# Optimization experiments

Measured on AMD Instinct MI355X. Metric: run time of the kernel, lower is better.

## Reference

```python
import jax, jax.numpy as jnp
import numpy as np

B, K, F_DIM, H_DIM, HEADS = 512, 17, 256, 256, 4
N = B * K           # 8704 flattened nodes
E = 139264          # edges (avg degree 16)
NEG_SLOPE = 0.2


def setup_inputs() -> dict:
    key = jax.random.key(0)
    ks = jax.random.split(key, 12)
    s_in = 1.0 / np.sqrt(F_DIM)
    s_hid = 1.0 / np.sqrt(H_DIM)
    return {
        "kpt_feature": jax.random.normal(ks[0], (B, K, F_DIM), jnp.float32),
        "edge_index": jax.random.randint(ks[1], (2, E), 0, N, jnp.int64),
        # conv1: F_DIM -> HEADS x H_DIM, concat=False (mean)
        "W1": jax.random.normal(ks[2], (F_DIM, HEADS * H_DIM), jnp.float32) * s_in,
        "a_src1": jax.random.normal(ks[3], (HEADS, H_DIM), jnp.float32) * s_hid,
        "a_dst1": jax.random.normal(ks[4], (HEADS, H_DIM), jnp.float32) * s_hid,
        "b1": jnp.zeros((H_DIM,), jnp.float32),
        # conv2: H_DIM -> HEADS x F_DIM, concat=False (mean)
        "W2": jax.random.normal(ks[5], (H_DIM, HEADS * F_DIM), jnp.float32) * s_hid,
        "a_src2": jax.random.normal(ks[6], (HEADS, F_DIM), jnp.float32) * s_in,
        "a_dst2": jax.random.normal(ks[7], (HEADS, F_DIM), jnp.float32) * s_in,
        "b2": jnp.zeros((F_DIM,), jnp.float32),
    }


def gat_conv(x, src, dst, W, a_src, a_dst, bias):
    # x: [N, Fin]; src/dst: [E'] (self-loops included); W: [Fin, H*C]
    n = x.shape[0]
    heads, c = a_src.shape
    h = (x @ W).reshape(n, heads, c)                       # [N,H,C]
    alpha_src = jnp.einsum("nhc,hc->nh", h, a_src)         # [N,H]
    alpha_dst = jnp.einsum("nhc,hc->nh", h, a_dst)
    e = jax.nn.leaky_relu(alpha_src[src] + alpha_dst[dst], NEG_SLOPE)  # [E',H]
    # segment softmax over incoming edges of each destination node
    emax = jax.ops.segment_max(e, dst, num_segments=n)
    emax = jnp.where(jnp.isfinite(emax), emax, 0.0)
    ex = jnp.exp(e - emax[dst])
    denom = jax.ops.segment_sum(ex, dst, num_segments=n)
    alpha = ex / denom[dst]                                # [E',H]
    msg = alpha[:, :, None] * h[src]                       # [E',H,C]
    out = jax.ops.segment_sum(msg, dst, num_segments=n)    # [N,H,C]
    return out.mean(axis=1) + bias                         # concat=False -> mean


def reference(kpt_feature, edge_index, W1, a_src1, a_dst1, b1, W2, a_src2, a_dst2, b2):
    b, k, f = kpt_feature.shape
    n = b * k
    x = kpt_feature.reshape(n, f)
    loop = jnp.arange(n, dtype=edge_index.dtype)
    src = jnp.concatenate([edge_index[0], loop])  # PyG add_self_loops=True
    dst = jnp.concatenate([edge_index[1], loop])
    x = gat_conv(x, src, dst, W1, a_src1, a_dst1, b1)
    x = jax.nn.relu(x)
    x = gat_conv(x, src, dst, W2, a_src2, a_dst2, b2)
    return x.reshape(b, k, f)
```

## Files before the change

### kernel.cpp

```cpp
#include <hip/hip_runtime.h>
#include <hip/hip_fp16.h>
#include <math.h>

#define NNODES 8704
#define NEDGE  139264
#define EPLUS  (NEDGE + NNODES)
#define NEG_SLOPE 0.2f
#define DEGCAP 64
#define LDSK   40

#define NB_PV  16
#define NB_WC  512
#define NB_SC  ((EPLUS + 255) / 256)
#define NB_AL  (NNODES / 4)

typedef _Float16 f16x8 __attribute__((ext_vector_type(8)));
typedef _Float16 f16x4 __attribute__((ext_vector_type(4)));
typedef float    f32x4 __attribute__((ext_vector_type(4)));

__device__ __forceinline__ float lrelu(float v) { return v >= 0.f ? v : NEG_SLOPE * v; }

__global__ __launch_bounds__(256) void prep_all(const float* __restrict__ W1,
                                                const float* __restrict__ as1,
                                                const float* __restrict__ ad1,
                                                const float* __restrict__ W2,
                                                const float* __restrict__ as2,
                                                const float* __restrict__ ad2,
                                                float* __restrict__ pbuf,
                                                int* __restrict__ cnt,
                                                float* __restrict__ alphasB,
                                                _Float16* __restrict__ Wc1,
                                                _Float16* __restrict__ Wc2) {
    __shared__ float tile[32][33];
    const int b = blockIdx.x;
    const int t = threadIdx.x;
    if (b < NB_PV) {
        for (int i = b * 256 + t; i < NNODES; i += NB_PV * 256) cnt[i] = 0;
        for (int i = b * 256 + t; i < NNODES * 8; i += NB_PV * 256) alphasB[i] = 0.f;
        float* a_sh = &tile[0][0];
        const int layer = b >> 3, sd = (b >> 2) & 1, h = b & 3;
        const float* W  = layer ? W2 : W1;
        const float* av = layer ? (sd ? ad2 : as2) : (sd ? ad1 : as1);
        a_sh[t] = av[h * 256 + t];
        __syncthreads();
        float acc = 0.f;
        const float* Wr = W + (size_t)t * 1024 + h * 256;
#pragma unroll 8
        for (int c = 0; c < 256; ++c) acc += Wr[c] * a_sh[c];
        pbuf[b * 256 + t] = acc;
    } else {
        const int idx = b - NB_PV;
        const int k0 = (idx & 7) * 32, o0 = ((idx >> 3) & 7) * 32;
        const int z = idx >> 6;
        const int layer = z >> 2, h = z & 3;
        const float* W = layer ? W2 : W1;
        _Float16* Wc   = layer ? Wc2 : Wc1;
#pragma unroll
        for (int p = 0; p < 4; ++p) {
            int e = t + p * 256; int kk = e >> 5, oo = e & 31;
            tile[kk][oo] = W[(size_t)(k0 + kk) * 1024 + h * 256 + o0 + oo];
        }
        __syncthreads();
#pragma unroll
        for (int p = 0; p < 4; ++p) {
            int e = t + p * 256; int oo = e >> 5, kk = e & 31;
            Wc[(size_t)(o0 + oo) * 1024 + h * 256 + k0 + kk] = (_Float16)tile[kk][oo];
        }
    }
}

__global__ __launch_bounds__(256) void scatter_alpha(const int* __restrict__ ei,
                                                     int* __restrict__ cnt,
                                                     int* __restrict__ csr,
                                                     const float* __restrict__ xf,
                                                     _Float16* __restrict__ xh_out,
                                                     const float* __restrict__ p ,
                                                     float* __restrict__ asrc,
                                                     float* __restrict__ adst) {
    const int b = blockIdx.x;
    const int t = threadIdx.x;
    if (b < NB_SC) {
        int e = b * 256 + t;
        if (e >= EPLUS) return;
        int src, dst;
        if (e < NEDGE) { src = ei[e]; dst = ei[NEDGE + e]; }
        else           { src = dst = e - NEDGE; }
        int slot = atomicAdd(&cnt[dst], 1);
        if (slot < DEGCAP) csr[dst * DEGCAP + slot] = src;
    } else {
        const int wave = t >> 6, l = t & 63;
        const int n = (b - NB_SC) * 4 + wave;
        float4 pv[8];
#pragma unroll
        for (int v = 0; v < 8; ++v) pv[v] = *(const float4*)(p + v * 256 + l * 4);
        float4 xv = *(const float4*)(xf + (size_t)n * 256 + l * 4);
        f16x4 hv = {(_Float16)xv.x, (_Float16)xv.y, (_Float16)xv.z, (_Float16)xv.w};
        *(f16x4*)(xh_out + (size_t)n * 256 + l * 4) = hv;
        float d[8];
#pragma unroll
        for (int v = 0; v < 8; ++v)
            d[v] = xv.x * pv[v].x + xv.y * pv[v].y + xv.z * pv[v].z + xv.w * pv[v].w;
#pragma unroll
        for (int off = 1; off <= 32; off <<= 1)
#pragma unroll
            for (int v = 0; v < 8; ++v) d[v] += __shfl_xor(d[v], off);
        if (l == 0) {
            *(float4*)(asrc + n * 4) = make_float4(d[0], d[1], d[2], d[3]);
            *(float4*)(adst + n * 4) = make_float4(d[4], d[5], d[6], d[7]);
        }
    }
}

__global__ __launch_bounds__(256) void agg_gather(const _Float16* __restrict__ xh,
                                                  const int* __restrict__ cnt,
                                                  const int* __restrict__ csr,
                                                  const float* __restrict__ asrc,
                                                  const float* __restrict__ adst,
                                                  _Float16* __restrict__ y) {
    const int w = threadIdx.x >> 6, l = threadIdx.x & 63;
    const int n = blockIdx.x * 4 + w;
    int deg = cnt[n]; if (deg > DEGCAP) deg = DEGCAP;

    float4 ad = *(const float4*)(adst + n * 4);
    int src_l = 0;
    float w0 = 0.f, w1 = 0.f, w2 = 0.f, w3 = 0.f;
    if (l < deg) {
        src_l = csr[n * DEGCAP + l];
        float4 as = *(const float4*)(asrc + src_l * 4);
        w0 = __expf(lrelu(as.x + ad.x));
        w1 = __expf(lrelu(as.y + ad.y));
        w2 = __expf(lrelu(as.z + ad.z));
        w3 = __expf(lrelu(as.w + ad.w));
    }
    float d0 = w0, d1 = w1, d2 = w2, d3 = w3;
#pragma unroll
    for (int off = 32; off >= 1; off >>= 1) {
        d0 += __shfl_xor(d0, off);
        d1 += __shfl_xor(d1, off);
        d2 += __shfl_xor(d2, off);
        d3 += __shfl_xor(d3, off);
    }
    w0 /= d0; w1 /= d1; w2 /= d2; w3 /= d3;

    float acc[4][4] = {};
    for (int s = 0; s < deg; ++s) {
        int src = __shfl(src_l, s);
        float u0 = __shfl(w0, s), u1 = __shfl(w1, s);
        float u2 = __shfl(w2, s), u3 = __shfl(w3, s);
        f16x4 xv = *(const f16x4*)(xh + (size_t)src * 256 + l * 4);
#pragma unroll
        for (int j = 0; j < 4; ++j) {
            float v = (float)xv[j];
            acc[j][0] += u0 * v; acc[j][1] += u1 * v;
            acc[j][2] += u2 * v; acc[j][3] += u3 * v;
        }
    }
#pragma unroll
    for (int h = 0; h < 4; ++h) {
        f16x4 pv = {(_Float16)acc[0][h], (_Float16)acc[1][h],
                    (_Float16)acc[2][h], (_Float16)acc[3][h]};
        *(f16x4*)(y + (size_t)n * 1024 + h * 256 + l * 4) = pv;
    }
}

__global__ __launch_bounds__(256) void gemm_out(const _Float16* __restrict__ Y,
                                                const _Float16* __restrict__ Wcatt,
                                                const float* __restrict__ bias,
                                                const float* __restrict__ p2,
                                                _Float16* __restrict__ outH,
                                                float* __restrict__ outF,
                                                float* __restrict__ asrc2,
                                                float* __restrict__ adst2) {
    __shared__ __align__(16) _Float16 As[64 * LDSK];
    __shared__ __align__(16) _Float16 Bs[256 * LDSK];
    __shared__ float p2s[8 * 256];
    const int t    = threadIdx.x;
    const int lane = t & 63;
    const int wave = t >> 6;
    const int wwr = wave >> 1, wwc = wave & 1;
    const int bm = blockIdx.x * 64;
    const int l15 = lane & 15, kb = lane >> 4;

    f32x4 acc[2][8] = {};

    int a_off[2], b_off[8];
#pragma unroll
    for (int i = 0; i < 2; ++i) a_off[i] = (wwr * 32 + i * 16 + l15) * LDSK + kb * 8;
#pragma unroll
    for (int j = 0; j < 8; ++j) b_off[j] = (wwc * 128 + j * 16 + l15) * LDSK + kb * 8;

    for (int k0 = 0; k0 < 1024; k0 += 32) {
        if (k0) __syncthreads();
        {
            int row = t >> 2, g = t & 3;
            f16x8 v = *(const f16x8*)(Y + (size_t)(bm + row) * 1024 + k0 + g * 8);
            *(f16x8*)(&As[row * LDSK + g * 8]) = v;
        }
#pragma unroll
        for (int p = 0; p < 4; ++p) {
            int e = t + p * 256;
            int row = e >> 2, g = e & 3;
            f16x8 v = *(const f16x8*)(Wcatt + (size_t)row * 1024 + k0 + g * 8);
            *(f16x8*)(&Bs[row * LDSK + g * 8]) = v;
        }
        __syncthreads();

        f16x8 af[2], bf[8];
#pragma unroll
        for (int i = 0; i < 2; ++i) af[i] = *(const f16x8*)(&As[a_off[i]]);
#pragma unroll
        for (int j = 0; j < 8; ++j) bf[j] = *(const f16x8*)(&Bs[b_off[j]]);
#pragma unroll
        for (int i = 0; i < 2; ++i)
#pragma unroll
            for (int j = 0; j < 8; ++j)
                acc[i][j] = __builtin_amdgcn_mfma_f32_16x16x32_f16(af[i], bf[j], acc[i][j], 0, 0, 0);
    }

    if (p2) {
#pragma unroll
        for (int v = 0; v < 8; ++v) p2s[v * 256 + t] = p2[v * 256 + t];
    }
    __syncthreads();

#pragma unroll
    for (int i = 0; i < 2; ++i)
#pragma unroll
        for (int q = 0; q < 4; ++q) {
            int row = bm + wwr * 32 + i * 16 + kb * 4 + q;
            float rv[8];
#pragma unroll
            for (int j = 0; j < 8; ++j) {
                int col = wwc * 128 + j * 16 + l15;
                float r = 0.25f * acc[i][j][q] + bias[col];
                rv[j] = r;
                if (outH) outH[(size_t)row * 256 + col] = (_Float16)fmaxf(r, 0.f);
                else      outF[(size_t)row * 256 + col] = r;
            }
            if (p2) {
#pragma unroll
                for (int v = 0; v < 8; ++v) {
                    float ps = 0.f;
#pragma unroll
                    for (int j = 0; j < 8; ++j) {
                        int col = wwc * 128 + j * 16 + l15;
                        ps += fmaxf(rv[j], 0.f) * p2s[v * 256 + col];
                    }
#pragma unroll
                    for (int off = 1; off <= 8; off <<= 1) ps += __shfl_xor(ps, off);
                    if (l15 == 0) {
                        if (v < 4) atomicAdd(&asrc2[row * 4 + v], ps);
                        else       atomicAdd(&adst2[row * 4 + (v - 4)], ps);
                    }
                }
            }
        }
}

extern "C" void kernel_launch(void* const* d_in, const int* in_sizes, int n_in,
                              void* d_out, int out_size, void* d_ws, size_t ws_size,
                              hipStream_t stream) {
    const float* x0  = (const float*)d_in[0];
    const int*   ei  = (const int*)d_in[1];
    const float* W1  = (const float*)d_in[2];
    const float* as1 = (const float*)d_in[3];
    const float* ad1 = (const float*)d_in[4];
    const float* b1  = (const float*)d_in[5];
    const float* W2  = (const float*)d_in[6];
    const float* as2 = (const float*)d_in[7];
    const float* ad2 = (const float*)d_in[8];
    const float* b2  = (const float*)d_in[9];
    float* out = (float*)d_out;

    char* w = (char*)d_ws;
    _Float16* y   = (_Float16*)w; w += (size_t)NNODES * 1024 * 2;
    _Float16* x0h = (_Float16*)w; w += (size_t)NNODES * 256 * 2;
    _Float16* x1h = (_Float16*)w; w += (size_t)NNODES * 256 * 2;
    _Float16* Wc1 = (_Float16*)w; w += (size_t)256 * 1024 * 2;
    _Float16* Wc2 = (_Float16*)w; w += (size_t)256 * 1024 * 2;
    float* pbuf   = (float*)w;    w += 16 * 256 * 4;
    float* asrcA  = (float*)w;    w += NNODES * 4 * 4;
    float* adstA  = (float*)w;    w += NNODES * 4 * 4;
    float* alphasB = (float*)w;   w += NNODES * 8 * 4;
    float* asrcB  = alphasB;
    float* adstB  = alphasB + NNODES * 4;
    int* cnt      = (int*)w;      w += NNODES * 4;
    int* csr      = (int*)w;      w += (size_t)NNODES * DEGCAP * 4;

    prep_all<<<NB_PV + NB_WC, 256, 0, stream>>>(W1, as1, ad1, W2, as2, ad2,
                                                pbuf, cnt, alphasB, Wc1, Wc2);
    scatter_alpha<<<NB_SC + NB_AL, 256, 0, stream>>>(ei, cnt, csr, x0, x0h, pbuf, asrcA, adstA);

    agg_gather<<<NNODES / 4, 256, 0, stream>>>(x0h, cnt, csr, asrcA, adstA, y);
    gemm_out<<<NNODES / 64, 256, 0, stream>>>(y, Wc1, b1, pbuf + 8 * 256, x1h, nullptr, asrcB, adstB);

    agg_gather<<<NNODES / 4, 256, 0, stream>>>(x1h, cnt, csr, asrcB, adstB, y);
    gemm_out<<<NNODES / 64, 256, 0, stream>>>(y, Wc2, b2, nullptr, nullptr, out, nullptr, nullptr);
}
```

Baseline: 142.3 us.

## Split output GEMM over column halves with 512-thread blocks and deeper K tile

The output GEMM grid gains a second dimension that splits the 256 output columns into two halves. Each block now runs 8 waves, and each wave computes a 32x32 tile instead of 32x128. The K step doubles to 64 with a padded LDS stride. The intent is to double block count (136 to 272) to fill more CUs and raise occupancy. The cost is that every Y tile is loaded twice and each wave gets less MFMA reuse per LDS load.

```diff
diff --git a/kernel.cpp b/kernel.cpp
--- a/kernel.cpp
+++ b/kernel.cpp
@@ -7,7 +7,7 @@
 #define EPLUS  (NEDGE + NNODES)
 #define NEG_SLOPE 0.2f
 #define DEGCAP 64
-#define LDSK   40
+#define LDSK2  72
 
 #define NB_PV  16
 #define NB_WC  512
@@ -163,7 +163,7 @@
     }
 }
 
-__global__ __launch_bounds__(256) void gemm_out(const _Float16* __restrict__ Y,
+__global__ __launch_bounds__(512) void gemm_out(const _Float16* __restrict__ Y,
                                                 const _Float16* __restrict__ Wcatt,
                                                 const float* __restrict__ bias,
                                                 const float* __restrict__ p2,
@@ -171,55 +171,63 @@
                                                 float* __restrict__ outF,
                                                 float* __restrict__ asrc2,
                                                 float* __restrict__ adst2) {
-    __shared__ __align__(16) _Float16 As[64 * LDSK];
-    __shared__ __align__(16) _Float16 Bs[256 * LDSK];
-    __shared__ float p2s[8 * 256];
+    __shared__ __align__(16) _Float16 As[64 * LDSK2];
+    __shared__ __align__(16) _Float16 Bs[128 * LDSK2];
+    __shared__ float p2s[8 * 128];
     const int t    = threadIdx.x;
     const int lane = t & 63;
     const int wave = t >> 6;
-    const int wwr = wave >> 1, wwc = wave & 1;
+    const int wwr = wave >> 2, wwc = wave & 3;
     const int bm = blockIdx.x * 64;
+    const int bn = blockIdx.y * 128;
     const int l15 = lane & 15, kb = lane >> 4;
 
-    f32x4 acc[2][8] = {};
-
-    int a_off[2], b_off[8];
-#pragma unroll
-    for (int i = 0; i < 2; ++i) a_off[i] = (wwr * 32 + i * 16 + l15) * LDSK + kb * 8;
-#pragma unroll
-    for (int j = 0; j < 8; ++j) b_off[j] = (wwc * 128 + j * 16 + l15) * LDSK + kb * 8;
-
-    for (int k0 = 0; k0 < 1024; k0 += 32) {
+    f32x4 acc[2][2] = {};
+
+    int a_off[2], b_off[2];
+#pragma unroll
+    for (int i = 0; i < 2; ++i) a_off[i] = (wwr * 32 + i * 16 + l15) * LDSK2 + kb * 8;
+#pragma unroll
+    for (int j = 0; j < 2; ++j) b_off[j] = (wwc * 32 + j * 16 + l15) * LDSK2 + kb * 8;
+
+    for (int k0 = 0; k0 < 1024; k0 += 64) {
         if (k0) __syncthreads();
         {
-            int row = t >> 2, g = t & 3;
+            int row = t >> 3, g = t & 7;
             f16x8 v = *(const f16x8*)(Y + (size_t)(bm + row) * 1024 + k0 + g * 8);
-            *(f16x8*)(&As[row * LDSK + g * 8]) = v;
-        }
-#pragma unroll
-        for (int p = 0; p < 4; ++p) {
-            int e = t + p * 256;
-            int row = e >> 2, g = e & 3;
-            f16x8 v = *(const f16x8*)(Wcatt + (size_t)row * 1024 + k0 + g * 8);
-            *(f16x8*)(&Bs[row * LDSK + g * 8]) = v;
+            *(f16x8*)(&As[row * LDSK2 + g * 8]) = v;
+        }
+#pragma unroll
+        for (int p = 0; p < 2; ++p) {
+            int e = t + p * 512;
+            int row = e >> 3, g = e & 7;
+            f16x8 v = *(const f16x8*)(Wcatt + (size_t)(bn + row) * 1024 + k0 + g * 8);
+            *(f16x8*)(&Bs[row * LDSK2 + g * 8]) = v;
         }
         __syncthreads();
 
-        f16x8 af[2], bf[8];
-#pragma unroll
-        for (int i = 0; i < 2; ++i) af[i] = *(const f16x8*)(&As[a_off[i]]);
-#pragma unroll
-        for (int j = 0; j < 8; ++j) bf[j] = *(const f16x8*)(&Bs[b_off[j]]);
-#pragma unroll
-        for (int i = 0; i < 2; ++i)
-#pragma unroll
-            for (int j = 0; j < 8; ++j)
-                acc[i][j] = __builtin_amdgcn_mfma_f32_16x16x32_f16(af[i], bf[j], acc[i][j], 0, 0, 0);
+#pragma unroll
+        for (int ks = 0; ks < 2; ++ks) {
+            f16x8 af[2], bf[2];
+#pragma unroll
+            for (int i = 0; i < 2; ++i) af[i] = *(const f16x8*)(&As[a_off[i] + ks * 32]);
+#pragma unroll
+            for (int j = 0; j < 2; ++j) bf[j] = *(const f16x8*)(&Bs[b_off[j] + ks * 32]);
+#pragma unroll
+            for (int i = 0; i < 2; ++i)
+#pragma unroll
+                for (int j = 0; j < 2; ++j)
+                    acc[i][j] = __builtin_amdgcn_mfma_f32_16x16x32_f16(af[i], bf[j], acc[i][j], 0, 0, 0);
+        }
     }
 
     if (p2) {
 #pragma unroll
-        for (int v = 0; v < 8; ++v) p2s[v * 256 + t] = p2[v * 256 + t];
+        for (int p = 0; p < 2; ++p) {
+            int e = t + p * 512;
+            int v = e >> 7, c = e & 127;
+            p2s[e] = p2[v * 256 + bn + c];
+        }
     }
     __syncthreads();
 
@@ -228,23 +236,23 @@
 #pragma unroll
         for (int q = 0; q < 4; ++q) {
             int row = bm + wwr * 32 + i * 16 + kb * 4 + q;
-            float rv[8];
-#pragma unroll
-            for (int j = 0; j < 8; ++j) {
-                int col = wwc * 128 + j * 16 + l15;
-                float r = 0.25f * acc[i][j][q] + bias[col];
+            float rv[2];
+#pragma unroll
+            for (int j = 0; j < 2; ++j) {
+                int cl = wwc * 32 + j * 16 + l15;
+                float r = 0.25f * acc[i][j][q] + bias[bn + cl];
                 rv[j] = r;
-                if (outH) outH[(size_t)row * 256 + col] = (_Float16)fmaxf(r, 0.f);
-                else      outF[(size_t)row * 256 + col] = r;
+                if (outH) outH[(size_t)row * 256 + bn + cl] = (_Float16)fmaxf(r, 0.f);
+                else      outF[(size_t)row * 256 + bn + cl] = r;
             }
             if (p2) {
 #pragma unroll
                 for (int v = 0; v < 8; ++v) {
                     float ps = 0.f;
 #pragma unroll
-                    for (int j = 0; j < 8; ++j) {
-                        int col = wwc * 128 + j * 16 + l15;
-                        ps += fmaxf(rv[j], 0.f) * p2s[v * 256 + col];
+                    for (int j = 0; j < 2; ++j) {
+                        int cl = wwc * 32 + j * 16 + l15;
+                        ps += fmaxf(rv[j], 0.f) * p2s[v * 128 + cl];
                     }
 #pragma unroll
                     for (int off = 1; off <= 8; off <<= 1) ps += __shfl_xor(ps, off);
@@ -287,13 +295,15 @@
     int* cnt      = (int*)w;      w += NNODES * 4;
     int* csr      = (int*)w;      w += (size_t)NNODES * DEGCAP * 4;
 
+    const dim3 gemm_grid(NNODES / 64, 2);
+
     prep_all<<<NB_PV + NB_WC, 256, 0, stream>>>(W1, as1, ad1, W2, as2, ad2,
                                                 pbuf, cnt, alphasB, Wc1, Wc2);
     scatter_alpha<<<NB_SC + NB_AL, 256, 0, stream>>>(ei, cnt, csr, x0, x0h, pbuf, asrcA, adstA);
 
     agg_gather<<<NNODES / 4, 256, 0, stream>>>(x0h, cnt, csr, asrcA, adstA, y);
-    gemm_out<<<NNODES / 64, 256, 0, stream>>>(y, Wc1, b1, pbuf + 8 * 256, x1h, nullptr, asrcB, adstB);
+    gemm_out<<<gemm_grid, 512, 0, stream>>>(y, Wc1, b1, pbuf + 8 * 256, x1h, nullptr, asrcB, adstB);
 
     agg_gather<<<NNODES / 4, 256, 0, stream>>>(x1h, cnt, csr, asrcB, adstB, y);
-    gemm_out<<<NNODES / 64, 256, 0, stream>>>(y, Wc2, b2, nullptr, nullptr, out, nullptr, nullptr);
-}
+    gemm_out<<<gemm_grid, 512, 0, stream>>>(y, Wc2, b2, nullptr, nullptr, out, nullptr, nullptr);
+}
```

Result: slower. 163.7 us (+15.1%).
